# Optimization experiments

Measured on AMD Instinct MI355X. Metric: run time of the kernel, lower is better.

The kernel has to match this reference:

```python
import jax, jax.numpy as jnp
import numpy as np

EPS_NORM = 1e-12  # torch F.normalize eps
EPS_LOG = 1e-6


def _l2_normalize(x, axis):
    n = jnp.linalg.norm(x, axis=axis, keepdims=True)
    return x / jnp.maximum(n, EPS_NORM)


def setup_inputs() -> dict:
    key = jax.random.key(0)
    k1, k2, k3 = jax.random.split(key, 3)
    B, C, D = 32, 5000, 512
    features = jax.random.normal(k1, (B, C, D), dtype=jnp.float32)
    embeddings = jax.random.normal(k2, (C, D), dtype=jnp.float32)
    labels = jax.random.randint(k3, (B, C), 0, 2).astype(jnp.float32)
    return {"features": features, "embeddings": embeddings, "labels": labels}


def reference(features, embeddings, labels):
    # features: (B, C, D), embeddings: (C, D), labels: (B, C)
    C = embeddings.shape[0]
    fn = _l2_normalize(features, axis=2)
    en = _l2_normalize(embeddings, axis=1)
    # diagonal of bmm(fn, en^T) == row-wise dot products: (B, C)
    similarities = jnp.einsum('bcd,cd->bc', fn, en)
    S = (1.0 + similarities) / 2.0 + EPS_LOG
    pos_loss = labels * jnp.log(S)
    neg_loss = (1.0 - labels) * jnp.log(
        1.0 - (C - 1) / C * jnp.abs(1.0 / (C - 1) + similarities) + EPS_LOG
    )
    return -(pos_loss + neg_loss).mean()
```

## Files before the change

kernel.cpp:

```cpp
#include <hip/hip_runtime.h>
#include <math.h>


constexpr int B = 32;
constexpr int C = 5000;
constexpr int D = 512;
constexpr int NROWS = B * C;
constexpr float EPS_NORM = 1e-12f;
constexpr float EPS_LOG = 1e-6f;

constexpr int WAVES_PER_C = 2;
constexpr int B_PER_WAVE = B / WAVES_PER_C;
constexpr int WPB = 4;
constexpr int MAIN_BLOCKS = C * WAVES_PER_C / WPB;
constexpr int THREADS = WPB * 64;

__global__ __launch_bounds__(THREADS) void fll_main(
    const float* __restrict__ feat,
    const float* __restrict__ emb,
    const float* __restrict__ labels,
    float* __restrict__ partial)
{
    const int lane = threadIdx.x & 63;
    const int wid  = threadIdx.x >> 6;
    const int gw   = blockIdx.x * WPB + wid;
    const int c    = gw >> 1;
    const int half = gw & 1;

    const float4* er = reinterpret_cast<const float4*>(emb + (size_t)c * D);
    const float4 e0 = er[lane];
    const float4 e1 = er[lane + 64];

    float ess = e0.x * e0.x + e0.y * e0.y + e0.z * e0.z + e0.w * e0.w
              + e1.x * e1.x + e1.y * e1.y + e1.z * e1.z + e1.w * e1.w;
    #pragma unroll
    for (int off = 32; off > 0; off >>= 1) ess += __shfl_xor(ess, off, 64);
    const float inv_ne = 1.0f / fmaxf(sqrtf(ess), EPS_NORM);

    const size_t bstride = (size_t)C * D;
    const float* fbase = feat + (size_t)(half * B_PER_WAVE) * bstride + (size_t)c * D;
    const float* lbase = labels + (size_t)(half * B_PER_WAVE) * C + c;

    float wacc = 0.0f;

    #pragma unroll 4
    for (int i = 0; i < B_PER_WAVE; ++i) {
        const float4* fr = reinterpret_cast<const float4*>(fbase + (size_t)i * bstride);
        const float4 f0 = fr[lane];
        const float4 f1 = fr[lane + 64];

        float dot = f0.x * e0.x + f0.y * e0.y + f0.z * e0.z + f0.w * e0.w
                  + f1.x * e1.x + f1.y * e1.y + f1.z * e1.z + f1.w * e1.w;
        float fss = f0.x * f0.x + f0.y * f0.y + f0.z * f0.z + f0.w * f0.w
                  + f1.x * f1.x + f1.y * f1.y + f1.z * f1.z + f1.w * f1.w;

        #pragma unroll
        for (int off = 32; off > 0; off >>= 1) {
            dot += __shfl_xor(dot, off, 64);
            fss += __shfl_xor(fss, off, 64);
        }

        const float inv_nf = 1.0f / fmaxf(sqrtf(fss), EPS_NORM);
        const float sim = dot * inv_nf * inv_ne;
        const float lab = lbase[(size_t)i * C];
        const float S = 0.5f * (1.0f + sim) + EPS_LOG;
        const float T = 1.0f
            - ((float)(C - 1) / (float)C) * fabsf(1.0f / (float)(C - 1) + sim)
            + EPS_LOG;
        wacc += logf(lab > 0.5f ? S : T);
    }

    __shared__ float wsum[WPB];
    if (lane == 0) wsum[wid] = wacc;
    __syncthreads();
    if (threadIdx.x == 0) {
        float s = 0.0f;
        #pragma unroll
        for (int w = 0; w < WPB; ++w) s += wsum[w];
        partial[blockIdx.x] = s;
    }
}

__global__ __launch_bounds__(THREADS) void fll_reduce(
    const float* __restrict__ partial, float* __restrict__ out)
{
    const int lane = threadIdx.x & 63;
    const int wave = threadIdx.x >> 6;
    double acc = 0.0;
    for (int i = threadIdx.x; i < MAIN_BLOCKS; i += THREADS) acc += (double)partial[i];

    #pragma unroll
    for (int off = 32; off > 0; off >>= 1) acc += __shfl_xor(acc, off, 64);

    __shared__ double s[THREADS / 64];
    if (lane == 0) s[wave] = acc;
    __syncthreads();
    if (threadIdx.x == 0) {
        double tot = 0.0;
        #pragma unroll
        for (int w = 0; w < THREADS / 64; ++w) tot += s[w];
        out[0] = (float)(-tot / (double)NROWS);
    }
}

extern "C" void kernel_launch(void* const* d_in, const int* in_sizes, int n_in,
                              void* d_out, int out_size, void* d_ws, size_t ws_size,
                              hipStream_t stream) {
    const float* feat   = (const float*)d_in[0];
    const float* emb    = (const float*)d_in[1];
    const float* labels = (const float*)d_in[2];
    float* out = (float*)d_out;
    float* partial = (float*)d_ws;

    fll_main<<<MAIN_BLOCKS, THREADS, 0, stream>>>(feat, emb, labels, partial);
    fll_reduce<<<1, THREADS, 0, stream>>>(partial, out);
}
```

Measured before the change: 65.19 us.

## Reassign waves to contiguous row segments per batch with nontemporal feature loads

Each wave now handles 25 consecutive c-rows within one batch instead of one c across 16 batches. Feature reads become contiguous streams and use nontemporal loads, while embedding rows are reloaded per row, likely from cache since all batches share them. The embedding norm is recomputed per row, and the two norms are merged into a single sqrt of the product, which drops the EPS_NORM clamp. The block size changes to 5 waves with an occupancy hint, and the reduce kernel gets a fixed 256-thread launch.

```diff
diff --git a/kernel.cpp b/kernel.cpp
--- a/kernel.cpp
+++ b/kernel.cpp
@@ -1,21 +1,23 @@
 #include <hip/hip_runtime.h>
 #include <math.h>
 
+
+typedef float f32x4 __attribute__((ext_vector_type(4)));
 
 constexpr int B = 32;
 constexpr int C = 5000;
 constexpr int D = 512;
 constexpr int NROWS = B * C;
-constexpr float EPS_NORM = 1e-12f;
 constexpr float EPS_LOG = 1e-6f;
 
-constexpr int WAVES_PER_C = 2;
-constexpr int B_PER_WAVE = B / WAVES_PER_C;
-constexpr int WPB = 4;
-constexpr int MAIN_BLOCKS = C * WAVES_PER_C / WPB;
+constexpr int ROWS_PER_WAVE = 25;
+constexpr int SEGS_PER_B = C / ROWS_PER_WAVE;
+constexpr int NWAVES = B * SEGS_PER_B;
+constexpr int WPB = 5;
 constexpr int THREADS = WPB * 64;
+constexpr int MAIN_BLOCKS = NWAVES / WPB;
 
-__global__ __launch_bounds__(THREADS) void fll_main(
+__global__ __launch_bounds__(THREADS, 7) void fll_main(
     const float* __restrict__ feat,
     const float* __restrict__ emb,
     const float* __restrict__ labels,
@@ -24,45 +26,40 @@
     const int lane = threadIdx.x & 63;
     const int wid  = threadIdx.x >> 6;
     const int gw   = blockIdx.x * WPB + wid;
-    const int c    = gw >> 1;
-    const int half = gw & 1;
+    const int b    = gw / SEGS_PER_B;
+    const int c0   = (gw % SEGS_PER_B) * ROWS_PER_WAVE;
 
-    const float4* er = reinterpret_cast<const float4*>(emb + (size_t)c * D);
-    const float4 e0 = er[lane];
-    const float4 e1 = er[lane + 64];
-
-    float ess = e0.x * e0.x + e0.y * e0.y + e0.z * e0.z + e0.w * e0.w
-              + e1.x * e1.x + e1.y * e1.y + e1.z * e1.z + e1.w * e1.w;
-    #pragma unroll
-    for (int off = 32; off > 0; off >>= 1) ess += __shfl_xor(ess, off, 64);
-    const float inv_ne = 1.0f / fmaxf(sqrtf(ess), EPS_NORM);
-
-    const size_t bstride = (size_t)C * D;
-    const float* fbase = feat + (size_t)(half * B_PER_WAVE) * bstride + (size_t)c * D;
-    const float* lbase = labels + (size_t)(half * B_PER_WAVE) * C + c;
+    const float* fbase = feat + ((size_t)b * C + c0) * D;
+    const float* ebase = emb + (size_t)c0 * D;
+    const float* lbase = labels + (size_t)b * C + c0;
 
     float wacc = 0.0f;
 
-    #pragma unroll 4
-    for (int i = 0; i < B_PER_WAVE; ++i) {
-        const float4* fr = reinterpret_cast<const float4*>(fbase + (size_t)i * bstride);
-        const float4 f0 = fr[lane];
-        const float4 f1 = fr[lane + 64];
+    #pragma unroll 2
+    for (int r = 0; r < ROWS_PER_WAVE; ++r) {
+        const f32x4* fr = reinterpret_cast<const f32x4*>(fbase + (size_t)r * D);
+        const f32x4* er = reinterpret_cast<const f32x4*>(ebase + (size_t)r * D);
+        const f32x4 f0 = __builtin_nontemporal_load(fr + lane);
+        const f32x4 f1 = __builtin_nontemporal_load(fr + lane + 64);
+        const f32x4 e0 = er[lane];
+        const f32x4 e1 = er[lane + 64];
 
         float dot = f0.x * e0.x + f0.y * e0.y + f0.z * e0.z + f0.w * e0.w
                   + f1.x * e1.x + f1.y * e1.y + f1.z * e1.z + f1.w * e1.w;
         float fss = f0.x * f0.x + f0.y * f0.y + f0.z * f0.z + f0.w * f0.w
                   + f1.x * f1.x + f1.y * f1.y + f1.z * f1.z + f1.w * f1.w;
+        float ess = e0.x * e0.x + e0.y * e0.y + e0.z * e0.z + e0.w * e0.w
+                  + e1.x * e1.x + e1.y * e1.y + e1.z * e1.z + e1.w * e1.w;
 
         #pragma unroll
         for (int off = 32; off > 0; off >>= 1) {
             dot += __shfl_xor(dot, off, 64);
             fss += __shfl_xor(fss, off, 64);
+            ess += __shfl_xor(ess, off, 64);
         }
 
-        const float inv_nf = 1.0f / fmaxf(sqrtf(fss), EPS_NORM);
-        const float sim = dot * inv_nf * inv_ne;
-        const float lab = lbase[(size_t)i * C];
+        const float sim = dot / sqrtf(fss * ess);
+        const float lab = lbase[r];
         const float S = 0.5f * (1.0f + sim) + EPS_LOG;
         const float T = 1.0f
             - ((float)(C - 1) / (float)C) * fabsf(1.0f / (float)(C - 1) + sim)
@@ -81,24 +78,24 @@
     }
 }
 
-__global__ __launch_bounds__(THREADS) void fll_reduce(
+__global__ __launch_bounds__(256) void fll_reduce(
     const float* __restrict__ partial, float* __restrict__ out)
 {
     const int lane = threadIdx.x & 63;
     const int wave = threadIdx.x >> 6;
     double acc = 0.0;
-    for (int i = threadIdx.x; i < MAIN_BLOCKS; i += THREADS) acc += (double)partial[i];
+    for (int i = threadIdx.x; i < MAIN_BLOCKS; i += 256) acc += (double)partial[i];
 
     #pragma unroll
     for (int off = 32; off > 0; off >>= 1) acc += __shfl_xor(acc, off, 64);
 
-    __shared__ double s[THREADS / 64];
+    __shared__ double s[4];
     if (lane == 0) s[wave] = acc;
     __syncthreads();
     if (threadIdx.x == 0) {
         double tot = 0.0;
         #pragma unroll
-        for (int w = 0; w < THREADS / 64; ++w) tot += s[w];
+        for (int w = 0; w < 4; ++w) tot += s[w];
         out[0] = (float)(-tot / (double)NROWS);
     }
 }
@@ -113,5 +110,5 @@
     float* partial = (float*)d_ws;
 
     fll_main<<<MAIN_BLOCKS, THREADS, 0, stream>>>(feat, emb, labels, partial);
-    fll_reduce<<<1, THREADS, 0, stream>>>(partial, out);
+    fll_reduce<<<1, 256, 0, stream>>>(partial, out);
 }
```

New measurement: 157.2 us. +141.2%, slower.
